# Kernel tuning notes

Measured on AMD Instinct MI355X. Metric: run time of the kernel, lower is better.

## Reference

```python
import jax, jax.numpy as jnp
import numpy as np

T_STEPS = 30
HIDDEN = 16
INPUT_DIM = 32
OUTPUT_DIM = 1
BATCH = 262144


def setup_inputs() -> dict:
    key = jax.random.key(0)
    ks = jax.random.split(key, 8)
    u = lambda k, shape: jax.random.uniform(k, shape, jnp.float32, -0.25, 0.25)
    return {
        "x": jax.random.normal(ks[0], (BATCH, INPUT_DIM), jnp.float32),
        "T": T_STEPS,
        "W_ih": u(ks[1], (HIDDEN, INPUT_DIM)),
        "W_hh": u(ks[2], (HIDDEN, HIDDEN)),
        "b_ih": u(ks[3], (HIDDEN,)),
        "b_hh": u(ks[4], (HIDDEN,)),
        "W_fc": jax.random.normal(ks[5], (OUTPUT_DIM, HIDDEN), jnp.float32) * 0.25,
        "b_fc": jax.random.normal(ks[6], (OUTPUT_DIM,), jnp.float32) * 0.25,
    }


def reference(x, T, W_ih, W_hh, b_ih, b_hh, W_fc, b_fc):
    # Input is the same at every timestep (x repeated T times), so the
    # input projection is computed once and reused across the scan.
    xproj = x @ W_ih.T + b_ih + b_hh  # [B, H]
    h0 = jnp.zeros((x.shape[0], W_hh.shape[0]), dtype=x.dtype)

    def step(h, _):
        h = jnp.tanh(xproj + h @ W_hh.T)  # Elman: tanh(Wx+b_ih + Uh+b_hh)
        return h, h

    _, hs = jax.lax.scan(step, h0, None, length=T)  # [T, B, H]
    hs = jnp.transpose(hs, (1, 0, 2))               # [B, T, H] (batch_first)
    return hs @ W_fc.T + b_fc                       # [B, T, output_dim]
```

## Files before the change

### kernel.cpp

```cpp
#include <hip/hip_runtime.h>


#define T_STEPS 30
#define BLOCK   256

typedef short v4s __attribute__((ext_vector_type(4)));
typedef float v4f __attribute__((ext_vector_type(4)));

__device__ __forceinline__ float tanh_fast(float v) {
    float e = __builtin_amdgcn_exp2f(v * 2.8853900817779268f);
    float r = __builtin_amdgcn_rcpf(1.0f + e);
    return fmaf(-2.0f, r, 1.0f);
}

__device__ __forceinline__ short bf16_trunc(float f) {
    return (short)(unsigned short)(__float_as_uint(f) >> 16);
}
__device__ __forceinline__ float bf16_trunc_f32(float f) {
    return __uint_as_float(__float_as_uint(f) & 0xFFFF0000u);
}

__global__ __launch_bounds__(BLOCK, 8) void rnn_mfma(
    const float* __restrict__ x,
    const float* __restrict__ W_ih,
    const float* __restrict__ W_hh,
    const float* __restrict__ b_ih,
    const float* __restrict__ b_hh,
    const float* __restrict__ W_fc,
    const float* __restrict__ b_fc,
    float* __restrict__ out)
{
    __shared__ float tmp[64 * T_STEPS];

    const int tid  = threadIdx.x;
    const int w    = tid >> 6;
    const int lane = tid & 63;
    const int r    = lane & 15;
    const int q    = lane >> 4;

    const size_t row = (size_t)blockIdx.x * 64 + (size_t)w * 16 + r;

    const int j0 = 4 * q;
    float xp0 = b_ih[j0 + 0] + b_hh[j0 + 0];
    float xp1 = b_ih[j0 + 1] + b_hh[j0 + 1];
    float xp2 = b_ih[j0 + 2] + b_hh[j0 + 2];
    float xp3 = b_ih[j0 + 3] + b_hh[j0 + 3];
    {
        const float4* xrow = (const float4*)(x + row * 32);
#pragma unroll
        for (int c4 = 0; c4 < 8; ++c4) {
            float4 xv = xrow[c4];
            const float4 w0 = *(const float4*)(W_ih + (j0 + 0) * 32 + c4 * 4);
            const float4 w1 = *(const float4*)(W_ih + (j0 + 1) * 32 + c4 * 4);
            const float4 w2 = *(const float4*)(W_ih + (j0 + 2) * 32 + c4 * 4);
            const float4 w3 = *(const float4*)(W_ih + (j0 + 3) * 32 + c4 * 4);
            xp0 = fmaf(w0.x, xv.x, fmaf(w0.y, xv.y, fmaf(w0.z, xv.z, fmaf(w0.w, xv.w, xp0))));
            xp1 = fmaf(w1.x, xv.x, fmaf(w1.y, xv.y, fmaf(w1.z, xv.z, fmaf(w1.w, xv.w, xp1))));
            xp2 = fmaf(w2.x, xv.x, fmaf(w2.y, xv.y, fmaf(w2.z, xv.z, fmaf(w2.w, xv.w, xp2))));
            xp3 = fmaf(w3.x, xv.x, fmaf(w3.y, xv.y, fmaf(w3.z, xv.z, fmaf(w3.w, xv.w, xp3))));
        }
    }
    v4f xpv = {xp0, xp1, xp2, xp3};

    float4 wrow = *(const float4*)(W_hh + r * 16 + 4 * q);
    v4s whi, wlo;
    {
        float wf[4] = {wrow.x, wrow.y, wrow.z, wrow.w};
#pragma unroll
        for (int i = 0; i < 4; ++i) {
            whi[i] = bf16_trunc(wf[i]);
            float lo = wf[i] - bf16_trunc_f32(wf[i]);
            wlo[i] = bf16_trunc(lo);
        }
    }

    const float4 wfc4 = *(const float4*)(W_fc + 4 * q);
    const float  bfc  = b_fc[0];

    v4s s_hi = {0, 0, 0, 0};
    v4s s_lo = {0, 0, 0, 0};

    for (int t = 0; t < T_STEPS; ++t) {
        v4f acc = __builtin_amdgcn_mfma_f32_16x16x16bf16_1k(whi, s_hi, xpv, 0, 0, 0);
        acc = __builtin_amdgcn_mfma_f32_16x16x16bf16_1k(whi, s_lo, acc, 0, 0, 0);
        acc = __builtin_amdgcn_mfma_f32_16x16x16bf16_1k(wlo, s_hi, acc, 0, 0, 0);

        float partial = 0.0f;
        const float wf[4] = {wfc4.x, wfc4.y, wfc4.z, wfc4.w};
#pragma unroll
        for (int i = 0; i < 4; ++i) {
            float h = tanh_fast(acc[i]);
            s_hi[i] = bf16_trunc(h);
            float lo = h - bf16_trunc_f32(h);
            s_lo[i] = bf16_trunc(lo);
            partial = fmaf(h, wf[i], partial);
        }

        partial += __shfl_xor(partial, 16);
        partial += __shfl_xor(partial, 32);

        if (lane < 16)
            tmp[(w * 16 + lane) * T_STEPS + t] = partial + bfc;
    }

    __syncthreads();

    float* oblk = out + (size_t)blockIdx.x * (64 * T_STEPS);
    for (int idx = tid; idx < 64 * T_STEPS; idx += BLOCK)
        oblk[idx] = tmp[idx];
}

extern "C" void kernel_launch(void* const* d_in, const int* in_sizes, int n_in,
                              void* d_out, int out_size, void* d_ws, size_t ws_size,
                              hipStream_t stream) {
    const float* x    = (const float*)d_in[0];
    const float* W_ih = (const float*)d_in[2];
    const float* W_hh = (const float*)d_in[3];
    const float* b_ih = (const float*)d_in[4];
    const float* b_hh = (const float*)d_in[5];
    const float* W_fc = (const float*)d_in[6];
    const float* b_fc = (const float*)d_in[7];
    float* out = (float*)d_out;

    const int B = in_sizes[0] / 32;
    const int grid = B / 64;

    rnn_mfma<<<grid, BLOCK, 0, stream>>>(x, W_ih, W_hh, b_ih, b_hh, W_fc, b_fc, out);
}
```

Before: 139.1 us.

## Compute FC projection with MFMA, pack bf16 via perm, unroll time loop

The output projection now runs on two extra MFMAs per step instead of per-lane FMAs plus two cross-lane shuffles. W_fc is split into hi and lo bf16 rows placed in A-matrix rows 0 and 1, and the bias is injected through the accumulator. bf16 packing uses v_perm to build two values per instruction, and the time loop is fully unrolled. This trades shuffle latency and ALU work for more MFMA issue on the serial dependency chain, and the FC product drops the lo*lo term, so precision shifts slightly.

```diff
diff --git a/kernel.cpp b/kernel.cpp
--- a/kernel.cpp
+++ b/kernel.cpp
@@ -6,6 +6,7 @@
 
 typedef short v4s __attribute__((ext_vector_type(4)));
 typedef float v4f __attribute__((ext_vector_type(4)));
+typedef int   v2i __attribute__((ext_vector_type(2)));
 
 __device__ __forceinline__ float tanh_fast(float v) {
     float e = __builtin_amdgcn_exp2f(v * 2.8853900817779268f);
@@ -13,9 +14,18 @@
     return fmaf(-2.0f, r, 1.0f);
 }
 
-__device__ __forceinline__ short bf16_trunc(float f) {
-    return (short)(unsigned short)(__float_as_uint(f) >> 16);
+__device__ __forceinline__ int pack_bf16hi(float a, float b) {
+    return (int)__builtin_amdgcn_perm(__float_as_uint(b), __float_as_uint(a),
+                                      0x07060302u);
 }
+
+__device__ __forceinline__ v4s pack4(float a, float b, float c, float d) {
+    v2i p;
+    p[0] = pack_bf16hi(a, b);
+    p[1] = pack_bf16hi(c, d);
+    return __builtin_bit_cast(v4s, p);
+}
+
 __device__ __forceinline__ float bf16_trunc_f32(float f) {
     return __uint_as_float(__float_as_uint(f) & 0xFFFF0000u);
 }
@@ -60,47 +70,56 @@
             xp3 = fmaf(w3.x, xv.x, fmaf(w3.y, xv.y, fmaf(w3.z, xv.z, fmaf(w3.w, xv.w, xp3))));
         }
     }
-    v4f xpv = {xp0, xp1, xp2, xp3};
+    const v4f xpv = {xp0, xp1, xp2, xp3};
 
-    float4 wrow = *(const float4*)(W_hh + r * 16 + 4 * q);
     v4s whi, wlo;
     {
-        float wf[4] = {wrow.x, wrow.y, wrow.z, wrow.w};
+        float4 wr = *(const float4*)(W_hh + r * 16 + 4 * q);
+        float wf[4] = {wr.x, wr.y, wr.z, wr.w};
+        whi = pack4(wf[0], wf[1], wf[2], wf[3]);
+        wlo = pack4(wf[0] - bf16_trunc_f32(wf[0]), wf[1] - bf16_trunc_f32(wf[1]),
+                    wf[2] - bf16_trunc_f32(wf[2]), wf[3] - bf16_trunc_f32(wf[3]));
+    }
+
+    v4s afc;
+    {
+        float f[4];
 #pragma unroll
         for (int i = 0; i < 4; ++i) {
-            whi[i] = bf16_trunc(wf[i]);
-            float lo = wf[i] - bf16_trunc_f32(wf[i]);
-            wlo[i] = bf16_trunc(lo);
+            float wv = W_fc[4 * q + i];
+            float lo = wv - bf16_trunc_f32(wv);
+            f[i] = (r == 0) ? wv : ((r == 1) ? lo : 0.0f);
         }
+        afc = pack4(f[0], f[1], f[2], f[3]);
     }
 
-    const float4 wfc4 = *(const float4*)(W_fc + 4 * q);
-    const float  bfc  = b_fc[0];
+    const float bfc = b_fc[0];
+    const v4f zfc = {(q == 0) ? bfc : 0.0f, 0.0f, 0.0f, 0.0f};
 
     v4s s_hi = {0, 0, 0, 0};
     v4s s_lo = {0, 0, 0, 0};
 
+    float* myout = &tmp[(w * 16 + r) * T_STEPS];
+
+#pragma unroll
     for (int t = 0; t < T_STEPS; ++t) {
         v4f acc = __builtin_amdgcn_mfma_f32_16x16x16bf16_1k(whi, s_hi, xpv, 0, 0, 0);
         acc = __builtin_amdgcn_mfma_f32_16x16x16bf16_1k(whi, s_lo, acc, 0, 0, 0);
         acc = __builtin_amdgcn_mfma_f32_16x16x16bf16_1k(wlo, s_hi, acc, 0, 0, 0);
 
-        float partial = 0.0f;
-        const float wf[4] = {wfc4.x, wfc4.y, wfc4.z, wfc4.w};
-#pragma unroll
-        for (int i = 0; i < 4; ++i) {
-            float h = tanh_fast(acc[i]);
-            s_hi[i] = bf16_trunc(h);
-            float lo = h - bf16_trunc_f32(h);
-            s_lo[i] = bf16_trunc(lo);
-            partial = fmaf(h, wf[i], partial);
-        }
+        float h0 = tanh_fast(acc[0]);
+        float h1 = tanh_fast(acc[1]);
+        float h2 = tanh_fast(acc[2]);
+        float h3 = tanh_fast(acc[3]);
+        s_hi = pack4(h0, h1, h2, h3);
+        s_lo = pack4(h0 - bf16_trunc_f32(h0), h1 - bf16_trunc_f32(h1),
+                     h2 - bf16_trunc_f32(h2), h3 - bf16_trunc_f32(h3));
 
-        partial += __shfl_xor(partial, 16);
-        partial += __shfl_xor(partial, 32);
+        v4f facc = __builtin_amdgcn_mfma_f32_16x16x16bf16_1k(afc, s_hi, zfc, 0, 0, 0);
+        facc = __builtin_amdgcn_mfma_f32_16x16x16bf16_1k(afc, s_lo, facc, 0, 0, 0);
 
         if (lane < 16)
-            tmp[(w * 16 + lane) * T_STEPS + t] = partial + bfc;
+            myout[t] = facc[0] + facc[1];
     }
 
     __syncthreads();
```

After: 138.6 us. No clear change (-0.3%).

## Replace split-bf16 triple MFMA recurrence with single fp16 MFMA and MFMA output projection

Applied to the files above, without the earlier changes.

Switches the recurrent matmul from three bf16 MFMAs (hi/lo split for near-fp32 accuracy) to one fp16 MFMA. The tanh exp2 scale factor is folded into W_hh and the input projection, which removes a multiply per element. The output projection moves from a per-lane FMA plus two cross-lane shuffles to a second MFMA that uses a hi/lo fp16 split of W_fc. The time loop is fully unrolled. This shortens the serial per-step dependency chain, but the hidden state is rounded toward zero to fp16 every step, and the scaled weights lose precision, so error can build up over 30 steps.

```diff
diff --git a/kernel.cpp b/kernel.cpp
--- a/kernel.cpp
+++ b/kernel.cpp
@@ -3,21 +3,18 @@
 
 #define T_STEPS 30
 #define BLOCK   256
+#define SCALE   2.8853900817779268f
 
-typedef short v4s __attribute__((ext_vector_type(4)));
-typedef float v4f __attribute__((ext_vector_type(4)));
+typedef _Float16 v4h __attribute__((ext_vector_type(4)));
+typedef __fp16   v2fp __attribute__((ext_vector_type(2)));
+typedef float    v4f __attribute__((ext_vector_type(4)));
 
-__device__ __forceinline__ float tanh_fast(float v) {
-    float e = __builtin_amdgcn_exp2f(v * 2.8853900817779268f);
+struct h4 { v2fp lo, hi; };
+
+__device__ __forceinline__ float tanh_pre(float a) {
+    float e = __builtin_amdgcn_exp2f(a);
     float r = __builtin_amdgcn_rcpf(1.0f + e);
     return fmaf(-2.0f, r, 1.0f);
-}
-
-__device__ __forceinline__ short bf16_trunc(float f) {
-    return (short)(unsigned short)(__float_as_uint(f) >> 16);
-}
-__device__ __forceinline__ float bf16_trunc_f32(float f) {
-    return __uint_as_float(__float_as_uint(f) & 0xFFFF0000u);
 }
 
 __global__ __launch_bounds__(BLOCK, 8) void rnn_mfma(
@@ -37,14 +34,14 @@
     const int lane = tid & 63;
     const int r    = lane & 15;
     const int q    = lane >> 4;
+    const int j0   = 4 * q;
 
     const size_t row = (size_t)blockIdx.x * 64 + (size_t)w * 16 + r;
 
-    const int j0 = 4 * q;
-    float xp0 = b_ih[j0 + 0] + b_hh[j0 + 0];
-    float xp1 = b_ih[j0 + 1] + b_hh[j0 + 1];
-    float xp2 = b_ih[j0 + 2] + b_hh[j0 + 2];
-    float xp3 = b_ih[j0 + 3] + b_hh[j0 + 3];
+    float a0 = b_ih[j0 + 0] + b_hh[j0 + 0];
+    float a1 = b_ih[j0 + 1] + b_hh[j0 + 1];
+    float a2 = b_ih[j0 + 2] + b_hh[j0 + 2];
+    float a3 = b_ih[j0 + 3] + b_hh[j0 + 3];
     {
         const float4* xrow = (const float4*)(x + row * 32);
 #pragma unroll
@@ -54,53 +51,56 @@
             const float4 w1 = *(const float4*)(W_ih + (j0 + 1) * 32 + c4 * 4);
             const float4 w2 = *(const float4*)(W_ih + (j0 + 2) * 32 + c4 * 4);
             const float4 w3 = *(const float4*)(W_ih + (j0 + 3) * 32 + c4 * 4);
-            xp0 = fmaf(w0.x, xv.x, fmaf(w0.y, xv.y, fmaf(w0.z, xv.z, fmaf(w0.w, xv.w, xp0))));
-            xp1 = fmaf(w1.x, xv.x, fmaf(w1.y, xv.y, fmaf(w1.z, xv.z, fmaf(w1.w, xv.w, xp1))));
-            xp2 = fmaf(w2.x, xv.x, fmaf(w2.y, xv.y, fmaf(w2.z, xv.z, fmaf(w2.w, xv.w, xp2))));
-            xp3 = fmaf(w3.x, xv.x, fmaf(w3.y, xv.y, fmaf(w3.z, xv.z, fmaf(w3.w, xv.w, xp3))));
+            a0 = fmaf(w0.x, xv.x, fmaf(w0.y, xv.y, fmaf(w0.z, xv.z, fmaf(w0.w, xv.w, a0))));
+            a1 = fmaf(w1.x, xv.x, fmaf(w1.y, xv.y, fmaf(w1.z, xv.z, fmaf(w1.w, xv.w, a1))));
+            a2 = fmaf(w2.x, xv.x, fmaf(w2.y, xv.y, fmaf(w2.z, xv.z, fmaf(w2.w, xv.w, a2))));
+            a3 = fmaf(w3.x, xv.x, fmaf(w3.y, xv.y, fmaf(w3.z, xv.z, fmaf(w3.w, xv.w, a3))));
         }
     }
-    v4f xpv = {xp0, xp1, xp2, xp3};
+    const v4f xpv = {a0 * SCALE, a1 * SCALE, a2 * SCALE, a3 * SCALE};
 
-    float4 wrow = *(const float4*)(W_hh + r * 16 + 4 * q);
-    v4s whi, wlo;
+    v4h whh;
     {
-        float wf[4] = {wrow.x, wrow.y, wrow.z, wrow.w};
-#pragma unroll
-        for (int i = 0; i < 4; ++i) {
-            whi[i] = bf16_trunc(wf[i]);
-            float lo = wf[i] - bf16_trunc_f32(wf[i]);
-            wlo[i] = bf16_trunc(lo);
-        }
+        float4 wr = *(const float4*)(W_hh + r * 16 + 4 * q);
+        whh[0] = (_Float16)(wr.x * SCALE);
+        whh[1] = (_Float16)(wr.y * SCALE);
+        whh[2] = (_Float16)(wr.z * SCALE);
+        whh[3] = (_Float16)(wr.w * SCALE);
     }
 
-    const float4 wfc4 = *(const float4*)(W_fc + 4 * q);
-    const float  bfc  = b_fc[0];
+    v4h afc;
+#pragma unroll
+    for (int i = 0; i < 4; ++i) {
+        float wv = W_fc[4 * q + i];
+        _Float16 hi = (_Float16)wv;
+        _Float16 lo = (_Float16)(wv - (float)hi);
+        afc[i] = (r == 0) ? hi : ((r == 1) ? lo : (_Float16)0.0f);
+    }
+    const float bfc = b_fc[0];
+    const v4f zfc = {(q == 0) ? bfc : 0.0f, 0.0f, 0.0f, 0.0f};
 
-    v4s s_hi = {0, 0, 0, 0};
-    v4s s_lo = {0, 0, 0, 0};
+    v4h s = {(_Float16)0.0f, (_Float16)0.0f, (_Float16)0.0f, (_Float16)0.0f};
 
+    float* myout = &tmp[(w * 16 + r) * T_STEPS];
+
+#pragma unroll
     for (int t = 0; t < T_STEPS; ++t) {
-        v4f acc = __builtin_amdgcn_mfma_f32_16x16x16bf16_1k(whi, s_hi, xpv, 0, 0, 0);
-        acc = __builtin_amdgcn_mfma_f32_16x16x16bf16_1k(whi, s_lo, acc, 0, 0, 0);
-        acc = __builtin_amdgcn_mfma_f32_16x16x16bf16_1k(wlo, s_hi, acc, 0, 0, 0);
+        v4f acc = __builtin_amdgcn_mfma_f32_16x16x16f16(whh, s, xpv, 0, 0, 0);
 
-        float partial = 0.0f;
-        const float wf[4] = {wfc4.x, wfc4.y, wfc4.z, wfc4.w};
-#pragma unroll
-        for (int i = 0; i < 4; ++i) {
-            float h = tanh_fast(acc[i]);
-            s_hi[i] = bf16_trunc(h);
-            float lo = h - bf16_trunc_f32(h);
-            s_lo[i] = bf16_trunc(lo);
-            partial = fmaf(h, wf[i], partial);
-        }
+        float h0 = tanh_pre(acc[0]);
+        float h1 = tanh_pre(acc[1]);
+        float h2 = tanh_pre(acc[2]);
+        float h3 = tanh_pre(acc[3]);
 
-        partial += __shfl_xor(partial, 16);
-        partial += __shfl_xor(partial, 32);
+        h4 p;
+        p.lo = __builtin_amdgcn_cvt_pkrtz(h0, h1);
+        p.hi = __builtin_amdgcn_cvt_pkrtz(h2, h3);
+        s = __builtin_bit_cast(v4h, p);
+
+        v4f f = __builtin_amdgcn_mfma_f32_16x16x16f16(afc, s, zfc, 0, 0, 0);
 
         if (lane < 16)
-            tmp[(w * 16 + lane) * T_STEPS + t] = partial + bfc;
+            myout[t] = f[0] + f[1];
     }
 
     __syncthreads();
```

New measurement: 131.2 us. 1.06x faster.
